# Kernel tuning notes

Hardware: AMD Instinct MI355X
Metric: run time of the kernel (lower is better)

## Reference

```python
import jax, jax.numpy as jnp
import numpy as np

N_NODES = 100_000
N_EDGES = 1_200_000
N_GRAPHS = 512
HID = 64


def setup_inputs() -> dict:
    key = jax.random.key(0)
    ks = jax.random.split(key, 8)
    x = jax.random.normal(ks[0], (N_NODES, 2), dtype=jnp.float32)
    edge_index = jax.random.randint(ks[1], (2, N_EDGES), 0, N_NODES, dtype=jnp.int32)
    batch = jnp.sort(jax.random.randint(ks[2], (N_NODES,), 0, N_GRAPHS, dtype=jnp.int32))
    def glorot(k, shape):
        fan_in, fan_out = shape
        s = jnp.sqrt(6.0 / (fan_in + fan_out))
        return jax.random.uniform(k, shape, jnp.float32, -s, s)
    return {
        "x": x, "edge_index": edge_index, "batch": batch, "num_graphs": N_GRAPHS,
        "W1": glorot(ks[3], (2, HID)), "b1": jnp.zeros((HID,), jnp.float32),
        "W2": glorot(ks[4], (HID, HID)), "b2": jnp.zeros((HID,), jnp.float32),
        "Wf1": glorot(ks[5], (HID, HID)), "bf1": jnp.zeros((HID,), jnp.float32),
        "Wf2": glorot(ks[6], (HID, 4)), "bf2": jnp.zeros((4,), jnp.float32),
    }


def gcn_conv(x, W, b, src, dst, n_nodes):
    """PyG GCNConv: sym-normalized A with self-loops, then linear."""
    h = x @ W  # [N, H] transform first (as PyG does)
    ones = jnp.ones(src.shape[0], x.dtype)
    deg = jax.ops.segment_sum(ones, dst, num_segments=n_nodes) + 1.0  # +1 self-loop
    dinv = jax.lax.rsqrt(deg)  # deg >= 1 always
    norm = dinv[src] * dinv[dst]  # [E]
    agg = jax.ops.segment_sum(h[src] * norm[:, None], dst, num_segments=n_nodes)
    agg = agg + h * (dinv * dinv)[:, None]  # self-loop contribution
    return agg + b


def global_mean_pool(x, batch, num_graphs):
    sums = jax.ops.segment_sum(x, batch, num_segments=num_graphs)
    cnts = jax.ops.segment_sum(jnp.ones(x.shape[0], x.dtype), batch, num_segments=num_graphs)
    return sums / jnp.maximum(cnts, 1.0)[:, None]


def reference(x, edge_index, batch, num_graphs, W1, b1, W2, b2, Wf1, bf1, Wf2, bf2):
    n = x.shape[0]
    src, dst = edge_index[0], edge_index[1]
    h = jax.nn.relu(gcn_conv(x, W1, b1, src, dst, n))   # dropout = identity (eval)
    h = jax.nn.relu(gcn_conv(h, W2, b2, src, dst, n))
    g = global_mean_pool(h, batch, num_graphs)          # [num_graphs, HID]
    g = jax.nn.relu(g @ Wf1 + bf1)
    return g @ Wf2 + bf2                                # [num_graphs, 4]
```

## Files before the change

### kernel.cpp

```cpp
#include <hip/hip_runtime.h>
#include <hip/hip_fp16.h>

#define NG 512
#define HID 64
#define CSH 9
#define BKT (1 << CSH)
#define PTILE 4096
#define MAXB 1024
#define TNB 128

__device__ __forceinline__ int pad8(int d) { return (d + 7) & ~7; }

__global__ __launch_bounds__(256) void partA_kernel(
    const int* __restrict__ src, const int* __restrict__ dst,
    const int* __restrict__ batch, int* __restrict__ gstart,
    int* __restrict__ bcnt, int* __restrict__ pstage,
    int E, int N, int nbc, int S) {
    __shared__ int hist[MAXB];
    __shared__ int base[MAXB];
    int tid = threadIdx.x;
    int t0 = blockIdx.x * PTILE;
    for (int i = blockIdx.x * 256 + tid; i < N; i += gridDim.x * 256) {
        int b = batch[i];
        int bp = (i == 0) ? -1 : batch[i - 1];
        for (int g = bp + 1; g <= b; ++g) gstart[g] = i;
        if (i == N - 1)
            for (int g = b + 1; g <= NG; ++g) gstart[g] = N;
    }
    for (int i = tid; i < nbc; i += 256) hist[i] = 0;
    __syncthreads();
    int es[PTILE / 256], ds[PTILE / 256];
#pragma unroll
    for (int j = 0; j < PTILE / 256; ++j) {
        int e = t0 + j * 256 + tid;
        if (e < E) {
            ds[j] = dst[e];
            es[j] = src[e];
            atomicAdd(&hist[ds[j] >> CSH], 1);
        } else {
            ds[j] = -1;
        }
    }
    __syncthreads();
    for (int i = tid; i < nbc; i += 256) {
        int c = hist[i];
        base[i] = c ? atomicAdd(&bcnt[i], c) : 0;
        hist[i] = 0;
    }
    __syncthreads();
#pragma unroll
    for (int j = 0; j < PTILE / 256; ++j) {
        if (ds[j] >= 0) {
            int b = ds[j] >> CSH;
            int r = base[b] + atomicAdd(&hist[b], 1);
            if (r < S)
                pstage[(size_t)b * S + r] = (es[j] << CSH) | (ds[j] & (BKT - 1));
        }
    }
}

__global__ __launch_bounds__(256) void partB2_kernel(
    const int* __restrict__ pstage, const int* __restrict__ bcnt,
    const float2* __restrict__ x2, int* __restrict__ deg, float* __restrict__ dinv,
    float2* __restrict__ xs2, int* __restrict__ rowbeg, int* __restrict__ esrc,
    int* __restrict__ ecur, __half* __restrict__ h2, int N, int S) {
    __shared__ int h[BKT];
    __shared__ int rowL[BKT];
    __shared__ int curL[BKT];
    __shared__ int ps[256];
    __shared__ int baseS;
    int c = blockIdx.x;
    int n0 = c << CSH;
    int tid = threadIdx.x;
    for (int i = tid; i < BKT; i += 256) h[i] = 0;
    __syncthreads();
    int cnt = min(bcnt[c], S);
    const int* pst = pstage + (size_t)c * S;
    for (int i = tid; i < cnt; i += 256) atomicAdd(&h[pst[i] & (BKT - 1)], 1);
    __syncthreads();
    int i0 = 2 * tid, i1 = 2 * tid + 1;
    int dg0 = (n0 + i0 < N) ? h[i0] : 0;
    int dg1 = (n0 + i1 < N) ? h[i1] : 0;
    if (n0 + i0 < N) {
        deg[n0 + i0] = dg0;
        float di = rsqrtf((float)dg0 + 1.0f);
        dinv[n0 + i0] = di;
        float2 xv = x2[n0 + i0];
        xs2[n0 + i0] = make_float2(xv.x * di, xv.y * di);
    }
    if (n0 + i1 < N) {
        deg[n0 + i1] = dg1;
        float di = rsqrtf((float)dg1 + 1.0f);
        dinv[n0 + i1] = di;
        float2 xv = x2[n0 + i1];
        xs2[n0 + i1] = make_float2(xv.x * di, xv.y * di);
    }
    int p0 = pad8(dg0), p1 = pad8(dg1);
    ps[tid] = p0 + p1;
    __syncthreads();
    for (int off = 1; off < 256; off <<= 1) {
        int t = (tid >= off) ? ps[tid - off] : 0;
        __syncthreads();
        ps[tid] += t;
        __syncthreads();
    }
    if (tid == 255) baseS = atomicAdd(ecur, ps[255]);
    __syncthreads();
    int excl = baseS + ps[tid] - (p0 + p1);
    rowL[i0] = excl;
    rowL[i1] = excl + p0;
    curL[i0] = 0;
    curL[i1] = 0;
    if (n0 + i0 < N) rowbeg[n0 + i0] = rowL[i0];
    if (n0 + i1 < N) rowbeg[n0 + i1] = rowL[i1];
    __syncthreads();
    for (int i = tid; i < cnt; i += 256) {
        int w = pst[i];
        int l = w & (BKT - 1);
        int p = rowL[l] + atomicAdd(&curL[l], 1);
        esrc[p] = w >> CSH;
    }
    __syncthreads();
    for (int l = tid; l < BKT; l += 256) {
        if (n0 + l < N) {
            int dg = curL[l];
            int p = rowL[l] + dg, p1e = rowL[l] + pad8(dg);
            for (; p < p1e; ++p) esrc[p] = N;
        }
    }
    if (c == 0) {
        if (tid == 0) xs2[N] = make_float2(0.0f, 0.0f);
        if (tid < 8)
            ((int4*)(h2 + (size_t)N * HID))[tid] = make_int4(0, 0, 0, 0);
    }
}

__global__ __launch_bounds__(256) void layer1a_kernel(
    const float2* __restrict__ xs2, const int* __restrict__ rowbeg,
    const int* __restrict__ deg, const int* __restrict__ esrc,
    const float* __restrict__ dinv, const float* __restrict__ W1,
    const float* __restrict__ b1, __half* __restrict__ h1s, int N) {
    int t = blockIdx.x * blockDim.x + threadIdx.x;
    int node = t >> 6, lane = t & 63;
    if (node >= N) return;
    int un = __builtin_amdgcn_readfirstlane(node);
    int k0 = __builtin_amdgcn_readfirstlane(rowbeg[un]);
    int k1 = k0 + pad8(__builtin_amdgcn_readfirstlane(deg[un]));
    float a0 = 0.0f, a1 = 0.0f;
    for (int e = k0; e < k1; e += 8) {
        const int4* ep = (const int4*)(esrc + e);
        int4 qa = ep[0], qb = ep[1];
        float2 v0 = xs2[qa.x], v1 = xs2[qa.y], v2 = xs2[qa.z], v3 = xs2[qa.w];
        float2 v4 = xs2[qb.x], v5 = xs2[qb.y], v6 = xs2[qb.z], v7 = xs2[qb.w];
        a0 += ((v0.x + v1.x) + (v2.x + v3.x)) + ((v4.x + v5.x) + (v6.x + v7.x));
        a1 += ((v0.y + v1.y) + (v2.y + v3.y)) + ((v4.y + v5.y) + (v6.y + v7.y));
    }
    float di = dinv[un];
    float2 xn = xs2[un];
    float m0 = di * (a0 + xn.x);
    float m1 = di * (a1 + xn.y);
    float v = fmaf(m0, W1[lane], fmaf(m1, W1[HID + lane], b1[lane]));
    h1s[(size_t)un * HID + lane] = __float2half_rn(fmaxf(v, 0.0f) * di);
}

__global__ __launch_bounds__(TNB) void l1gemm_kernel(
    const __half* __restrict__ h1s, const float* __restrict__ W2,
    __half* __restrict__ h2, int N) {
    __shared__ float h1t[HID * TNB];
    int t = threadIdx.x;
    int node0 = blockIdx.x * TNB;
    const int4* g4 = (const int4*)h1s;
#pragma unroll
    for (int r = 0; r < 8; ++r) {
        int g = r * TNB + t;
        int nd = g >> 3, kq = g & 7;
        int4 v = make_int4(0, 0, 0, 0);
        if (node0 + nd < N) v = g4[(size_t)(node0 + nd) * 8 + kq];
        const __half* hp = (const __half*)&v;
        int kb = kq * 8;
#pragma unroll
        for (int u = 0; u < 8; ++u)
            h1t[(kb + u) * TNB + (nd ^ ((kb + u) & 31))] = __half2float(hp[u]);
    }
    __syncthreads();
    int node = node0 + t;
    bool alive = node < N;
#pragma unroll 1
    for (int jt = 0; jt < 8; ++jt) {
        float c0 = 0.f, c1 = 0.f, c2 = 0.f, c3 = 0.f;
        float c4 = 0.f, c5 = 0.f, c6 = 0.f, c7 = 0.f;
#pragma unroll 8
        for (int k = 0; k < HID; ++k) {
            float h = h1t[k * TNB + (t ^ (k & 31))];
            const float4* wr = (const float4*)(W2 + k * HID + jt * 8);
            float4 wa = wr[0], wb = wr[1];
            c0 = fmaf(h, wa.x, c0); c1 = fmaf(h, wa.y, c1);
            c2 = fmaf(h, wa.z, c2); c3 = fmaf(h, wa.w, c3);
            c4 = fmaf(h, wb.x, c4); c5 = fmaf(h, wb.y, c5);
            c6 = fmaf(h, wb.z, c6); c7 = fmaf(h, wb.w, c7);
        }
        if (alive) {
            union { __half h[8]; int4 v; } u;
            u.h[0] = __float2half_rn(c0); u.h[1] = __float2half_rn(c1);
            u.h[2] = __float2half_rn(c2); u.h[3] = __float2half_rn(c3);
            u.h[4] = __float2half_rn(c4); u.h[5] = __float2half_rn(c5);
            u.h[6] = __float2half_rn(c6); u.h[7] = __float2half_rn(c7);
            *(int4*)(h2 + (size_t)node * HID + jt * 8) = u.v;
        }
    }
}

__global__ __launch_bounds__(256, 8) void layer2_kernel(
    const int* __restrict__ rowbeg, const int* __restrict__ deg,
    const int* __restrict__ esrc, const float* __restrict__ dinv,
    const __half* __restrict__ h2, const float* __restrict__ b2,
    const int* __restrict__ batch, float* __restrict__ gsum, int N) {
    int lane = threadIdx.x & 63;
    float bz = b2[lane];
    int wave = (blockIdx.x * 256 + threadIdx.x) >> 6;
    int nwaves = gridDim.x * 4;
    int npw = (N + nwaves - 1) / nwaves;
    int nA = wave * npw;
    int nB = min(N, nA + npw);
    int gcur = -1;
    float zacc = 0.0f;
    for (int node = nA; node < nB; ++node) {
        int un = __builtin_amdgcn_readfirstlane(node);
        int k0 = __builtin_amdgcn_readfirstlane(rowbeg[un]);
        int k1 = k0 + pad8(__builtin_amdgcn_readfirstlane(deg[un]));
        float acc = __half2float(h2[(un << 6) + lane]);
        int e = k0;
        for (; e + 32 <= k1; e += 32) {
            const int4* ep = (const int4*)(esrc + e);
            int4 q0 = ep[0], q1 = ep[1], q2 = ep[2], q3 = ep[3];
            int4 q4 = ep[4], q5 = ep[5], q6 = ep[6], q7 = ep[7];
            float r0  = __half2float(h2[(q0.x << 6) + lane]);
            float r1  = __half2float(h2[(q0.y << 6) + lane]);
            float r2  = __half2float(h2[(q0.z << 6) + lane]);
            float r3  = __half2float(h2[(q0.w << 6) + lane]);
            float r4  = __half2float(h2[(q1.x << 6) + lane]);
            float r5  = __half2float(h2[(q1.y << 6) + lane]);
            float r6  = __half2float(h2[(q1.z << 6) + lane]);
            float r7  = __half2float(h2[(q1.w << 6) + lane]);
            float r8  = __half2float(h2[(q2.x << 6) + lane]);
            float r9  = __half2float(h2[(q2.y << 6) + lane]);
            float r10 = __half2float(h2[(q2.z << 6) + lane]);
            float r11 = __half2float(h2[(q2.w << 6) + lane]);
            float r12 = __half2float(h2[(q3.x << 6) + lane]);
            float r13 = __half2float(h2[(q3.y << 6) + lane]);
            float r14 = __half2float(h2[(q3.z << 6) + lane]);
            float r15 = __half2float(h2[(q3.w << 6) + lane]);
            float r16 = __half2float(h2[(q4.x << 6) + lane]);
            float r17 = __half2float(h2[(q4.y << 6) + lane]);
            float r18 = __half2float(h2[(q4.z << 6) + lane]);
            float r19 = __half2float(h2[(q4.w << 6) + lane]);
            float r20 = __half2float(h2[(q5.x << 6) + lane]);
            float r21 = __half2float(h2[(q5.y << 6) + lane]);
            float r22 = __half2float(h2[(q5.z << 6) + lane]);
            float r23 = __half2float(h2[(q5.w << 6) + lane]);
            float r24 = __half2float(h2[(q6.x << 6) + lane]);
            float r25 = __half2float(h2[(q6.y << 6) + lane]);
            float r26 = __half2float(h2[(q6.z << 6) + lane]);
            float r27 = __half2float(h2[(q6.w << 6) + lane]);
            float r28 = __half2float(h2[(q7.x << 6) + lane]);
            float r29 = __half2float(h2[(q7.y << 6) + lane]);
            float r30 = __half2float(h2[(q7.z << 6) + lane]);
            float r31 = __half2float(h2[(q7.w << 6) + lane]);
            acc += ((((r0 + r1) + (r2 + r3)) + ((r4 + r5) + (r6 + r7)))
                  + (((r8 + r9) + (r10 + r11)) + ((r12 + r13) + (r14 + r15))))
                 + ((((r16 + r17) + (r18 + r19)) + ((r20 + r21) + (r22 + r23)))
                  + (((r24 + r25) + (r26 + r27)) + ((r28 + r29) + (r30 + r31))));
        }
        if (e + 16 <= k1) {
            const int4* ep = (const int4*)(esrc + e);
            int4 qa = ep[0], qb = ep[1], qc = ep[2], qd = ep[3];
            float r0 = __half2float(h2[(qa.x << 6) + lane]);
            float r1 = __half2float(h2[(qa.y << 6) + lane]);
            float r2 = __half2float(h2[(qa.z << 6) + lane]);
            float r3 = __half2float(h2[(qa.w << 6) + lane]);
            float r4 = __half2float(h2[(qb.x << 6) + lane]);
            float r5 = __half2float(h2[(qb.y << 6) + lane]);
            float r6 = __half2float(h2[(qb.z << 6) + lane]);
            float r7 = __half2float(h2[(qb.w << 6) + lane]);
            float r8 = __half2float(h2[(qc.x << 6) + lane]);
            float r9 = __half2float(h2[(qc.y << 6) + lane]);
            float r10 = __half2float(h2[(qc.z << 6) + lane]);
            float r11 = __half2float(h2[(qc.w << 6) + lane]);
            float r12 = __half2float(h2[(qd.x << 6) + lane]);
            float r13 = __half2float(h2[(qd.y << 6) + lane]);
            float r14 = __half2float(h2[(qd.z << 6) + lane]);
            float r15 = __half2float(h2[(qd.w << 6) + lane]);
            acc += (((r0 + r1) + (r2 + r3)) + ((r4 + r5) + (r6 + r7)))
                 + (((r8 + r9) + (r10 + r11)) + ((r12 + r13) + (r14 + r15)));
            e += 16;
        }
        if (e < k1) {
            const int4* ep = (const int4*)(esrc + e);
            int4 qa = ep[0], qb = ep[1];
            float r0 = __half2float(h2[(qa.x << 6) + lane]);
            float r1 = __half2float(h2[(qa.y << 6) + lane]);
            float r2 = __half2float(h2[(qa.z << 6) + lane]);
            float r3 = __half2float(h2[(qa.w << 6) + lane]);
            float r4 = __half2float(h2[(qb.x << 6) + lane]);
            float r5 = __half2float(h2[(qb.y << 6) + lane]);
            float r6 = __half2float(h2[(qb.z << 6) + lane]);
            float r7 = __half2float(h2[(qb.w << 6) + lane]);
            acc += ((r0 + r1) + (r2 + r3)) + ((r4 + r5) + (r6 + r7));
        }
        float z = fmaxf(fmaf(dinv[un], acc, bz), 0.0f);
        int g = __builtin_amdgcn_readfirstlane(batch[un]);
        if (g != gcur) {
            if (gcur >= 0) atomicAdd(&gsum[(gcur << 6) + lane], zacc);
            gcur = g;
            zacc = 0.0f;
        }
        zacc += z;
    }
    if (gcur >= 0) atomicAdd(&gsum[(gcur << 6) + lane], zacc);
}

__global__ void head_kernel(const float* __restrict__ gsum, const int* __restrict__ gstart,
                            const float* __restrict__ Wf1, const float* __restrict__ bf1,
                            const float* __restrict__ Wf2, const float* __restrict__ bf2,
                            float* __restrict__ out) {
    __shared__ float gs[HID];
    __shared__ float ts[HID];
    int b = blockIdx.x;
    int j = threadIdx.x;
    float cnt = fmaxf((float)(gstart[b + 1] - gstart[b]), 1.0f);
    gs[j] = gsum[b * HID + j] / cnt;
    __syncthreads();
    float acc = bf1[j];
#pragma unroll
    for (int k = 0; k < HID; ++k) acc = fmaf(gs[k], Wf1[k * HID + j], acc);
    ts[j] = fmaxf(acc, 0.0f);
    __syncthreads();
    if (j < 4) {
        float o = bf2[j];
#pragma unroll
        for (int k = 0; k < HID; ++k) o = fmaf(ts[k], Wf2[k * 4 + j], o);
        out[b * 4 + j] = o;
    }
}

extern "C" void kernel_launch(void* const* d_in, const int* in_sizes, int n_in,
                              void* d_out, int out_size, void* d_ws, size_t ws_size,
                              hipStream_t stream) {
    const float* x   = (const float*)d_in[0];
    const int*   ei  = (const int*)d_in[1];
    const int*   bat = (const int*)d_in[2];
    const float* W1  = (const float*)d_in[4];
    const float* b1  = (const float*)d_in[5];
    const float* W2  = (const float*)d_in[6];
    const float* b2  = (const float*)d_in[7];
    const float* Wf1 = (const float*)d_in[8];
    const float* bf1 = (const float*)d_in[9];
    const float* Wf2 = (const float*)d_in[10];
    const float* bf2 = (const float*)d_in[11];
    float* out = (float*)d_out;

    int N = in_sizes[2];
    int E = in_sizes[1] / 2;
    const int* src = ei;
    const int* dst = ei + E;
    int nbc = (N + BKT - 1) >> CSH;
    int ntile = (E + PTILE - 1) / PTILE;
    int S = 2 * (E / nbc) + 1024;
    size_t Ecap = ((size_t)E + 7 * (size_t)N + 8 + 3) & ~(size_t)3;

    char* ws = (char*)d_ws;
    size_t off = 0;
    auto alloc = [&](size_t bytes) {
        char* p = ws + off;
        off = (off + bytes + 255) & ~(size_t)255;
        return p;
    };
    int*    bcnt   = (int*)alloc((size_t)MAXB * 4);
    int*    ecur   = (int*)alloc(256);
    float*  gsum   = (float*)alloc((size_t)NG * HID * 4);
    int*    deg    = (int*)alloc((size_t)N * 4);
    float*  dinv   = (float*)alloc((size_t)N * 4);
    int*    rowbeg = (int*)alloc((size_t)N * 4);
    int*    esrc   = (int*)alloc(Ecap * 4);
    int*    pstage = (int*)alloc((size_t)nbc * S * 4);
    float2* xs2    = (float2*)alloc((size_t)(N + 1) * 8);
    __half* h1buf  = (__half*)alloc((size_t)N * HID * 2);
    __half* h2buf  = (__half*)alloc((size_t)(N + 1) * HID * 2);
    int*    gstart = (int*)alloc((size_t)(NG + 1) * 4);

    hipMemsetAsync(bcnt, 0, (size_t)((char*)gsum - (char*)bcnt) + (size_t)NG * HID * 4,
                   stream);

    partA_kernel<<<ntile, 256, 0, stream>>>(src, dst, bat, gstart, bcnt, pstage, E, N,
                                            nbc, S);
    partB2_kernel<<<nbc, 256, 0, stream>>>(pstage, bcnt, (const float2*)x, deg, dinv, xs2,
                                           rowbeg, esrc, ecur, h2buf, N, S);

    int nh = N * HID;
    layer1a_kernel<<<(nh + 255) / 256, 256, 0, stream>>>(xs2, rowbeg, deg, esrc, dinv, W1,
                                                         b1, h1buf, N);
    l1gemm_kernel<<<(N + TNB - 1) / TNB, TNB, 0, stream>>>(h1buf, W2, h2buf, N);

    layer2_kernel<<<4096, 256, 0, stream>>>(rowbeg, deg, esrc, dinv, h2buf, b2, bat, gsum,
                                            N);

    head_kernel<<<NG, HID, 0, stream>>>(gsum, gstart, Wf1, bf1, Wf2, bf2, out);
}
```

Baseline: 222.7 us.

## Store layer-1 aggregate as float4 and recompute hidden layer inside GEMM kernel

Layer-1 aggregation now writes only the two aggregated features plus dinv per node (16 bytes) instead of a 64-wide half hidden vector. The GEMM kernel recomputes the 64-wide relu(xW1+b1)*dinv in registers per thread and drops the shared-memory transpose staging. This removes the 12.8 MB h1 write and read round trip and the LDS traffic. In exchange it adds a 64-float register array per thread, which may spill or lower occupancy, and repeats the W1 evaluation in every thread.

```diff
diff --git a/kernel.cpp b/kernel.cpp
--- a/kernel.cpp
+++ b/kernel.cpp
@@ -7,7 +7,6 @@
 #define BKT (1 << CSH)
 #define PTILE 4096
 #define MAXB 1024
-#define TNB 128
 
 __device__ __forceinline__ int pad8(int d) { return (d + 7) & ~7; }
 
@@ -138,8 +137,7 @@
 __global__ __launch_bounds__(256) void layer1a_kernel(
     const float2* __restrict__ xs2, const int* __restrict__ rowbeg,
     const int* __restrict__ deg, const int* __restrict__ esrc,
-    const float* __restrict__ dinv, const float* __restrict__ W1,
-    const float* __restrict__ b1, __half* __restrict__ h1s, int N) {
+    const float* __restrict__ dinv, float4* __restrict__ agg, int N) {
     int t = blockIdx.x * blockDim.x + threadIdx.x;
     int node = t >> 6, lane = t & 63;
     if (node >= N) return;
@@ -155,43 +153,36 @@
         a0 += ((v0.x + v1.x) + (v2.x + v3.x)) + ((v4.x + v5.x) + (v6.x + v7.x));
         a1 += ((v0.y + v1.y) + (v2.y + v3.y)) + ((v4.y + v5.y) + (v6.y + v7.y));
     }
-    float di = dinv[un];
-    float2 xn = xs2[un];
-    float m0 = di * (a0 + xn.x);
-    float m1 = di * (a1 + xn.y);
-    float v = fmaf(m0, W1[lane], fmaf(m1, W1[HID + lane], b1[lane]));
-    h1s[(size_t)un * HID + lane] = __float2half_rn(fmaxf(v, 0.0f) * di);
-}
-
-__global__ __launch_bounds__(TNB) void l1gemm_kernel(
-    const __half* __restrict__ h1s, const float* __restrict__ W2,
+    if (lane == 0) {
+        float di = dinv[un];
+        float2 xn = xs2[un];
+        float m0 = di * (a0 + xn.x);
+        float m1 = di * (a1 + xn.y);
+        agg[un] = make_float4(m0, m1, di, 0.0f);
+    }
+}
+
+__global__ __launch_bounds__(256) void l1gemm_kernel(
+    const float4* __restrict__ agg, const float* __restrict__ W1,
+    const float* __restrict__ b1, const float* __restrict__ W2,
     __half* __restrict__ h2, int N) {
-    __shared__ float h1t[HID * TNB];
-    int t = threadIdx.x;
-    int node0 = blockIdx.x * TNB;
-    const int4* g4 = (const int4*)h1s;
-#pragma unroll
-    for (int r = 0; r < 8; ++r) {
-        int g = r * TNB + t;
-        int nd = g >> 3, kq = g & 7;
-        int4 v = make_int4(0, 0, 0, 0);
-        if (node0 + nd < N) v = g4[(size_t)(node0 + nd) * 8 + kq];
-        const __half* hp = (const __half*)&v;
-        int kb = kq * 8;
-#pragma unroll
-        for (int u = 0; u < 8; ++u)
-            h1t[(kb + u) * TNB + (nd ^ ((kb + u) & 31))] = __half2float(hp[u]);
-    }
-    __syncthreads();
-    int node = node0 + t;
-    bool alive = node < N;
+    int node = blockIdx.x * 256 + threadIdx.x;
+    if (node >= N) return;
+    float4 af = agg[node];
+    float m0 = af.x, m1 = af.y, di = af.z;
+    float h1r[HID];
+#pragma unroll
+    for (int k = 0; k < HID; ++k) {
+        float v = fmaf(m0, W1[k], fmaf(m1, W1[HID + k], b1[k]));
+        h1r[k] = fmaxf(v, 0.0f) * di;
+    }
 #pragma unroll 1
     for (int jt = 0; jt < 8; ++jt) {
         float c0 = 0.f, c1 = 0.f, c2 = 0.f, c3 = 0.f;
         float c4 = 0.f, c5 = 0.f, c6 = 0.f, c7 = 0.f;
-#pragma unroll 8
+#pragma unroll
         for (int k = 0; k < HID; ++k) {
-            float h = h1t[k * TNB + (t ^ (k & 31))];
+            float h = h1r[k];
             const float4* wr = (const float4*)(W2 + k * HID + jt * 8);
             float4 wa = wr[0], wb = wr[1];
             c0 = fmaf(h, wa.x, c0); c1 = fmaf(h, wa.y, c1);
@@ -199,14 +190,12 @@
             c4 = fmaf(h, wb.x, c4); c5 = fmaf(h, wb.y, c5);
             c6 = fmaf(h, wb.z, c6); c7 = fmaf(h, wb.w, c7);
         }
-        if (alive) {
-            union { __half h[8]; int4 v; } u;
-            u.h[0] = __float2half_rn(c0); u.h[1] = __float2half_rn(c1);
-            u.h[2] = __float2half_rn(c2); u.h[3] = __float2half_rn(c3);
-            u.h[4] = __float2half_rn(c4); u.h[5] = __float2half_rn(c5);
-            u.h[6] = __float2half_rn(c6); u.h[7] = __float2half_rn(c7);
-            *(int4*)(h2 + (size_t)node * HID + jt * 8) = u.v;
-        }
+        union { __half h[8]; int4 v; } u;
+        u.h[0] = __float2half_rn(c0); u.h[1] = __float2half_rn(c1);
+        u.h[2] = __float2half_rn(c2); u.h[3] = __float2half_rn(c3);
+        u.h[4] = __float2half_rn(c4); u.h[5] = __float2half_rn(c5);
+        u.h[6] = __float2half_rn(c6); u.h[7] = __float2half_rn(c7);
+        *(int4*)(h2 + (size_t)node * HID + jt * 8) = u.v;
     }
 }
 
@@ -384,7 +373,7 @@
     int*    esrc   = (int*)alloc(Ecap * 4);
     int*    pstage = (int*)alloc((size_t)nbc * S * 4);
     float2* xs2    = (float2*)alloc((size_t)(N + 1) * 8);
-    __half* h1buf  = (__half*)alloc((size_t)N * HID * 2);
+    float4* aggbuf = (float4*)alloc((size_t)N * 16);
     __half* h2buf  = (__half*)alloc((size_t)(N + 1) * HID * 2);
     int*    gstart = (int*)alloc((size_t)(NG + 1) * 4);
 
@@ -397,9 +386,9 @@
                                            rowbeg, esrc, ecur, h2buf, N, S);
 
     int nh = N * HID;
-    layer1a_kernel<<<(nh + 255) / 256, 256, 0, stream>>>(xs2, rowbeg, deg, esrc, dinv, W1,
-                                                         b1, h1buf, N);
-    l1gemm_kernel<<<(N + TNB - 1) / TNB, TNB, 0, stream>>>(h1buf, W2, h2buf, N);
+    layer1a_kernel<<<(nh + 255) / 256, 256, 0, stream>>>(xs2, rowbeg, deg, esrc, dinv,
+                                                         aggbuf, N);
+    l1gemm_kernel<<<(N + 255) / 256, 256, 0, stream>>>(aggbuf, W1, b1, W2, h2buf, N);
 
     layer2_kernel<<<4096, 256, 0, stream>>>(rowbeg, deg, esrc, dinv, h2buf, b2, bat, gsum,
                                             N);
```

New measurement: 307.4 us. 1.38x slower.
